# Performance work log

Hardware: AMD Instinct MI355X
Metric: run time of the kernel (lower is better)

The kernel has to match this reference:

```python
import jax, jax.numpy as jnp
import numpy as np

DIM = 512
HEADS = 8
DH = DIM // HEADS          # 64
M = DIM // 2               # 256 landmarks
ITERS = 6
KSZ = 33                   # residual depthwise conv kernel
LN_EPS = 1e-5
SCALE = DH ** -0.5


def setup_inputs() -> dict:
    key = jax.random.key(0)
    ks = jax.random.split(key, 5)
    b, n = 2, 8192
    x = jax.random.normal(ks[0], (b, n, DIM), jnp.float32)
    ln_g = jnp.ones((DIM,), jnp.float32)
    ln_b = jnp.zeros((DIM,), jnp.float32)
    sc = 1.0 / np.sqrt(DIM)
    W_qkv = (jax.random.normal(ks[1], (DIM, 3 * DIM), jnp.float32) * sc)
    W_out = (jax.random.normal(ks[2], (DIM, DIM), jnp.float32) * sc)
    b_out = jnp.zeros((DIM,), jnp.float32)
    conv_w = jax.random.normal(ks[3], (HEADS, 1, KSZ, 1), jnp.float32) * (1.0 / np.sqrt(KSZ))
    return dict(x=x, ln_g=ln_g, ln_b=ln_b, W_qkv=W_qkv, W_out=W_out, b_out=b_out, conv_w=conv_w)


def _pinv_iter(a, iters=ITERS):
    # Moore-Penrose pseudo-inverse via Newton-Schulz (lucidrains variant)
    abs_a = jnp.abs(a)
    col = abs_a.sum(-1)
    row = abs_a.sum(-2)
    z = jnp.swapaxes(a, -1, -2) / (jnp.max(col) * jnp.max(row))
    I = jnp.eye(a.shape[-1], dtype=a.dtype)
    for _ in range(iters):
        az = a @ z
        z = 0.25 * z @ (13 * I - az @ (15 * I - az @ (7 * I - az)))
    return z


def _nystrom_attention(xn, W_qkv, conv_w, W_out, b_out):
    b, n, _ = xn.shape
    qkv = xn @ W_qkv                                   # [b,n,3*dim]
    q, k, v = jnp.split(qkv, 3, axis=-1)
    to_heads = lambda t: t.reshape(b, n, HEADS, DH).transpose(0, 2, 1, 3)  # [b,h,n,d]
    q, k, v = to_heads(q), to_heads(k), to_heads(v)
    q = q * SCALE

    # landmarks: mean over contiguous groups of size l = n // M (n divisible by M)
    l = n // M
    q_l = q.reshape(b, HEADS, M, l, DH).sum(3) / l     # [b,h,M,d]
    k_l = k.reshape(b, HEADS, M, l, DH).sum(3) / l

    sim1 = jnp.einsum('bhnd,bhmd->bhnm', q, k_l)       # [b,h,n,M]
    sim2 = jnp.einsum('bhid,bhjd->bhij', q_l, k_l)     # [b,h,M,M]
    sim3 = jnp.einsum('bhmd,bhnd->bhmn', q_l, k)       # [b,h,M,n]

    attn1 = jax.nn.softmax(sim1, axis=-1)
    attn2 = jax.nn.softmax(sim2, axis=-1)
    attn3 = jax.nn.softmax(sim3, axis=-1)
    attn2_inv = _pinv_iter(attn2)

    out = (attn1 @ attn2_inv) @ (attn3 @ v)            # [b,h,n,d]

    # depthwise conv residual over sequence dim, per head (Conv2d kernel (33,1), groups=heads)
    pad = KSZ // 2
    res = jax.lax.conv_general_dilated(
        v, conv_w, window_strides=(1, 1), padding=((pad, pad), (0, 0)),
        dimension_numbers=('NCHW', 'OIHW', 'NCHW'), feature_group_count=HEADS)
    out = out + res

    out = out.transpose(0, 2, 1, 3).reshape(b, n, DIM)
    return out @ W_out + b_out


def reference(x, ln_g, ln_b, W_qkv, W_out, b_out, conv_w):
    mu = x.mean(-1, keepdims=True)
    var = x.var(-1, keepdims=True)
    xn = (x - mu) / jnp.sqrt(var + LN_EPS) * ln_g + ln_b
    return xn + _nystrom_attention(xn, W_qkv, conv_w, W_out, b_out)
```

## Files before the change

kernel.cpp:

```cpp
#include <hip/hip_runtime.h>

typedef unsigned short u16;
typedef short bh8 __attribute__((ext_vector_type(8)));
typedef float f32x4 __attribute__((ext_vector_type(4)));

#define NSEQ 8192
#define ALOFF 1048576
#define KVLOFF 262144
#define NSPLIT 8

__device__ __forceinline__ float b2f(u16 u){
  union { unsigned int u32; float f; } v; v.u32 = ((unsigned int)u) << 16; return v.f;
}
__device__ __forceinline__ u16 f2b(float f){
  union { float f; unsigned int u32; } v; v.f = f;
  unsigned int r = (v.u32 + 0x7FFFu + ((v.u32 >> 16) & 1u)) >> 16;
  return (u16)r;
}
__device__ __forceinline__ void glds16(const u16* g, u16* l){
  __builtin_amdgcn_global_load_lds((const __attribute__((address_space(1))) unsigned int*)g,
                                   (__attribute__((address_space(3))) unsigned int*)l, 16, 0, 0);
}

__global__ __launch_bounds__(256) void setup_kernel(const void* g, const void* bta, const void* bo,
                                                    const void* cw, const void* wq, const void* wo,
                                                    u16* gb, u16* bb, u16* bob, u16* cwb,
                                                    u16* wqt, u16* wot,
                                                    unsigned* flag, float* colsum){
  int f32 = (((const u16*)g)[0] != 0x3F80u);
  long tid = (long)blockIdx.x*256 + threadIdx.x;
  long nth = (long)gridDim.x*256;
  if(tid==0){ *flag = (unsigned)f32; }
  for(long i=tid;i<4096;i+=nth) colsum[i]=0.f;
  for(long i=tid;i<512;i+=nth) gb[i]  = f32 ? f2b(((const float*)g)[i])   : ((const u16*)g)[i];
  for(long i=tid;i<512;i+=nth) bb[i]  = f32 ? f2b(((const float*)bta)[i]) : ((const u16*)bta)[i];
  for(long i=tid;i<512;i+=nth) bob[i] = f32 ? f2b(((const float*)bo)[i])  : ((const u16*)bo)[i];
  for(long i=tid;i<264;i+=nth) cwb[i] = f32 ? f2b(((const float*)cw)[i])  : ((const u16*)cw)[i];
  for(long i=tid;i<786432;i+=nth){
    long n = i>>9, k = i&511;
    wqt[i] = f32 ? f2b(((const float*)wq)[k*1536+n]) : ((const u16*)wq)[k*1536+n];
  }
  for(long i=tid;i<262144;i+=nth){
    long n = i>>9, k = i&511;
    wot[i] = f32 ? f2b(((const float*)wo)[k*512+n]) : ((const u16*)wo)[k*512+n];
  }
}

__global__ __launch_bounds__(256) void ln_kernel(const void* xv, const unsigned* flag,
                                                 const u16* g, const u16* bta, u16* xn){
  int f32 = (*flag != 0u);
  long base = (long)blockIdx.x * 512;
  int t = threadIdx.x;
  float v0, v1;
  if(f32){ v0 = ((const float*)xv)[base+t]; v1 = ((const float*)xv)[base+256+t]; }
  else   { v0 = b2f(((const u16*)xv)[base+t]); v1 = b2f(((const u16*)xv)[base+256+t]); }
  float s = v0 + v1, sq = v0*v0 + v1*v1;
  #pragma unroll
  for(int k=1;k<64;k<<=1){ s += __shfl_xor(s,k,64); sq += __shfl_xor(sq,k,64); }
  __shared__ float s4[4], q4[4];
  if((t&63)==0){ s4[t>>6]=s; q4[t>>6]=sq; }
  __syncthreads();
  s = s4[0]+s4[1]+s4[2]+s4[3];
  sq = q4[0]+q4[1]+q4[2]+q4[3];
  float mu = s * (1.f/512.f);
  float var = sq * (1.f/512.f) - mu*mu;
  float inv = rsqrtf(var + 1e-5f);
  xn[base + t]       = f2b((v0-mu)*inv*b2f(g[t])     + b2f(bta[t]));
  xn[base + 256 + t] = f2b((v1-mu)*inv*b2f(g[t+256]) + b2f(bta[t+256]));
}

struct G128 {
  const u16 *A, *Bt; u16* C;
  const u16 *bias, *resid;
  const unsigned* oflag;
  int lda, ldb, ldc, ldr, K;
};
__global__ __launch_bounds__(256) void gemm128_kernel(G128 p){
  __shared__ u16 Ah[128][32];
  __shared__ u16 Bh[128][32];
  int t = threadIdx.x;
  int n0 = blockIdx.x*128, m0 = blockIdx.y*128;
  int w = t>>6, lane = t&63, l15 = lane&15, quad = lane>>4;
  int mw = (w>>1)*64, nw = (w&1)*64;
  int srow = lane>>2;
  int schunk = ((lane&3) ^ ((srow>>1)&3))*8;
  int cs = (quad ^ ((l15>>1)&3))*8;
  f32x4 acc[4][4];
  #pragma unroll
  for(int i=0;i<4;i++)
    #pragma unroll
    for(int j=0;j<4;j++)
      #pragma unroll
      for(int k=0;k<4;k++) acc[i][j][k]=0.f;

  for(int kk=0; kk<p.K; kk+=32){
    __syncthreads();
    glds16(p.A  + (long)(m0+32*w+srow)*p.lda    + kk + schunk, &Ah[32*w][0]);
    glds16(p.A  + (long)(m0+32*w+16+srow)*p.lda + kk + schunk, &Ah[32*w+16][0]);
    glds16(p.Bt + (long)(n0+32*w+srow)*p.ldb    + kk + schunk, &Bh[32*w][0]);
    glds16(p.Bt + (long)(n0+32*w+16+srow)*p.ldb + kk + schunk, &Bh[32*w+16][0]);
    __syncthreads();
    bh8 av[4], bv[4];
    #pragma unroll
    for(int mi=0;mi<4;mi++) av[mi] = *(const bh8*)&Ah[mw + mi*16 + l15][cs];
    #pragma unroll
    for(int ni=0;ni<4;ni++) bv[ni] = *(const bh8*)&Bh[nw + ni*16 + l15][cs];
    #pragma unroll
    for(int mi=0;mi<4;mi++)
      #pragma unroll
      for(int ni=0;ni<4;ni++)
        acc[mi][ni] = __builtin_amdgcn_mfma_f32_16x16x32_bf16(av[mi], bv[ni], acc[mi][ni], 0,0,0);
  }
  int f32o = p.oflag ? (int)(*p.oflag) : 0;
  #pragma unroll
  for(int mi=0;mi<4;mi++)
    #pragma unroll
    for(int ni=0;ni<4;ni++)
      #pragma unroll
      for(int r=0;r<4;r++){
        int row = m0 + mw + mi*16 + quad*4 + r;
        int col = n0 + nw + ni*16 + l15;
        float v = acc[mi][ni][r];
        if(p.bias)  v += b2f(p.bias[col]);
        if(p.resid) v += b2f(p.resid[(long)row*p.ldr + col]);
        long coff = (long)row*p.ldc + col;
        if(p.oflag){
          if(f32o) ((float*)p.C)[coff] = v; else p.C[coff] = f2b(v);
        } else p.C[coff] = f2b(v);
      }
}

__global__ __launch_bounds__(64) void landmark_kernel(const u16* qkv, u16* ql, u16* kl){
  int m = blockIdx.x, bh = blockIdx.y;
  int b = bh>>3, h = bh&7;
  int d = threadIdx.x;
  long base = ((long)b*NSEQ + (long)m*32)*1536 + h*64 + d;
  float sq=0.f, sk=0.f;
  for(int i=0;i<32;i++){
    sq += b2f(qkv[base + (long)i*1536]);
    sk += b2f(qkv[base + (long)i*1536 + 512]);
  }
  long o = ((long)bh*256 + m)*64 + d;
  ql[o] = f2b(sq * (1.f/32.f) * 0.125f);
  kl[o] = f2b(sk * (1.f/32.f));
}

__global__ __launch_bounds__(256) void sim2_kernel(const u16* ql, const u16* kl,
                                                   u16* ab, float* colsum){
  int mt = blockIdx.x, bh = blockIdx.y;
  __shared__ u16 qlds[64][72];
  __shared__ u16 klds[256][72];
  int t = threadIdx.x, w = t>>6, lane = t&63, l15 = lane&15, quad = lane>>4;
  {
    int r = t>>2, c = (t&3)*16;
    const u16* src = ql + (long)bh*16384 + (long)(mt*64 + r)*64 + c;
    *(uint4*)&qlds[r][c]   = *(const uint4*)src;
    *(uint4*)&qlds[r][c+8] = *(const uint4*)(src+8);
    #pragma unroll
    for(int pss=0; pss<4; pss++){
      int kr = pss*64 + r;
      const u16* ks = kl + (long)bh*16384 + (long)kr*64 + c;
      *(uint4*)&klds[kr][c]   = *(const uint4*)ks;
      *(uint4*)&klds[kr][c+8] = *(const uint4*)(ks+8);
    }
  }
  __syncthreads();
  f32x4 acc[16];
  #pragma unroll
  for(int i=0;i<16;i++)
    #pragma unroll
    for(int j=0;j<4;j++) acc[i][j]=0.f;
  #pragma unroll
  for(int g=0; g<16; g++)
    #pragma unroll
    for(int kk=0; kk<64; kk+=32){
      bh8 a  = *(const bh8*)&qlds[w*16+l15][kk+quad*8];
      bh8 bb = *(const bh8*)&klds[g*16+l15][kk+quad*8];
      acc[g] = __builtin_amdgcn_mfma_f32_16x16x32_bf16(a, bb, acc[g], 0,0,0);
    }
  #pragma unroll
  for(int r=0;r<4;r++){
    float m = -3.0e38f;
    #pragma unroll
    for(int g=0;g<16;g++) m = fmaxf(m, acc[g][r]);
    #pragma unroll
    for(int k=1;k<16;k<<=1) m = fmaxf(m, __shfl_xor(m,k,16));
    float s = 0.f;
    #pragma unroll
    for(int g=0;g<16;g++){ float e = __expf(acc[g][r]-m); acc[g][r]=e; s+=e; }
    #pragma unroll
    for(int k=1;k<16;k<<=1) s += __shfl_xor(s,k,16);
    float inv = 1.f/s;
    #pragma unroll
    for(int g=0;g<16;g++) acc[g][r] *= inv;
  }
  long bbase = (long)bh*65536;
  #pragma unroll
  for(int g=0;g<16;g++){
    float ps = 0.f;
    #pragma unroll
    for(int r=0;r<4;r++){
      int row = mt*64 + w*16 + quad*4 + r;
      int col = g*16 + l15;
      float pv = acc[g][r];
      u16 h = f2b(pv);
      ab[bbase + (long)row*256 + col] = h;
      ab[ALOFF + bbase + (long)row*256 + col] = f2b(pv - b2f(h));
      ps += pv;
    }
    ps += __shfl_xor(ps, 16);
    ps += __shfl_xor(ps, 32);
    if(quad==0) atomicAdd(&colsum[bh*256 + g*16 + l15], ps);
  }
}

__global__ __launch_bounds__(256) void pinv_init_kernel(const u16* ah, const float* colsum, u16* zh){
  int tile = blockIdx.x, bh = blockIdx.y;
  int tx = tile&3, ty = tile>>2;
  __shared__ u16 th[64][72], tl[64][72];
  __shared__ float red[4];
  int t = threadIdx.x;
  float mc = 0.f;
  for(int i=t;i<4096;i+=256) mc = fmaxf(mc, colsum[i]);
  #pragma unroll
  for(int k=1;k<64;k<<=1) mc = fmaxf(mc, __shfl_xor(mc,k,64));
  if((t&63)==0) red[t>>6]=mc;
  int r = t>>2, c = (t&3)*16;
  const u16* src = ah + (long)bh*65536 + (long)(ty*64 + r)*256 + tx*64 + c;
  *(uint4*)&th[r][c]   = *(const uint4*)src;
  *(uint4*)&th[r][c+8] = *(const uint4*)(src+8);
  *(uint4*)&tl[r][c]   = *(const uint4*)(src+ALOFF);
  *(uint4*)&tl[r][c+8] = *(const uint4*)(src+ALOFF+8);
  __syncthreads();
  float dinv = 1.f/fmaxf(fmaxf(red[0],red[1]), fmaxf(red[2],red[3]));
  u16 oh[16], ol[16];
  #pragma unroll
  for(int jj=0;jj<16;jj++){
    float v = (b2f(th[c+jj][r]) + b2f(tl[c+jj][r])) * dinv;
    u16 h = f2b(v);
    oh[jj] = h; ol[jj] = f2b(v - b2f(h));
  }
  u16* dst = zh + (long)bh*65536 + (long)(tx*64 + r)*256 + ty*64 + c;
  *(uint4*)dst     = *(uint4*)oh;
  *(uint4*)(dst+8) = *(uint4*)(oh+8);
  *(uint4*)(dst+ALOFF)   = *(uint4*)ol;
  *(uint4*)(dst+ALOFF+8) = *(uint4*)(ol+8);
}

struct NSG { const u16 *A, *B; u16 *Ch, *Cl, *C2h, *C2l; float alpha, beta, alpha2, beta2; };
__global__ __launch_bounds__(256) void ns_gemm_kernel(NSG p){
  __shared__ u16 Ah[64][40], Al[64][40], Bh[64][40], Bl[64][40];
  int t = threadIdx.x;
  long boff = (long)blockIdx.z*65536;
  int n0 = blockIdx.x*64, m0 = blockIdx.y*64;
  int w = t>>6, lane = t&63, l15 = lane&15, quad = lane>>4;
  int ar = t>>2, ac = (t&3)*8;
  int bk = t>>3, bn = (t&7)*8;
  f32x4 acc[4];
  #pragma unroll
  for(int i=0;i<4;i++)
    #pragma unroll
    for(int j=0;j<4;j++) acc[i][j]=0.f;
  for(int kk=0; kk<256; kk+=32){
    __syncthreads();
    *(uint4*)&Ah[ar][ac] = *(const uint4*)(p.A + boff + (long)(m0+ar)*256 + kk + ac);
    *(uint4*)&Al[ar][ac] = *(const uint4*)(p.A + ALOFF + boff + (long)(m0+ar)*256 + kk + ac);
    u16 th[8], tl[8];
    *(uint4*)th = *(const uint4*)(p.B + boff + (long)(kk+bk)*256 + n0 + bn);
    *(uint4*)tl = *(const uint4*)(p.B + ALOFF + boff + (long)(kk+bk)*256 + n0 + bn);
    #pragma unroll
    for(int j=0;j<8;j++){ Bh[bn+j][bk] = th[j]; Bl[bn+j][bk] = tl[j]; }
    __syncthreads();
    bh8 a  = *(const bh8*)&Ah[w*16+l15][quad*8];
    bh8 al = *(const bh8*)&Al[w*16+l15][quad*8];
    #pragma unroll
    for(int ct=0; ct<4; ct++){
      bh8 b  = *(const bh8*)&Bh[ct*16+l15][quad*8];
      bh8 bl = *(const bh8*)&Bl[ct*16+l15][quad*8];
      acc[ct] = __builtin_amdgcn_mfma_f32_16x16x32_bf16(a,  b,  acc[ct], 0,0,0);
      acc[ct] = __builtin_amdgcn_mfma_f32_16x16x32_bf16(a,  bl, acc[ct], 0,0,0);
      acc[ct] = __builtin_amdgcn_mfma_f32_16x16x32_bf16(al, b,  acc[ct], 0,0,0);
    }
  }
  #pragma unroll
  for(int ct=0; ct<4; ct++)
    #pragma unroll
    for(int r=0;r<4;r++){
      int col = n0 + ct*16 + l15;
      int row = m0 + w*16 + quad*4 + r;
      long coff = boff + (long)row*256 + col;
      float v = acc[ct][r];
      float v1 = p.alpha*v + ((row==col) ? p.beta : 0.f);
      u16 h = f2b(v1);
      p.Ch[coff] = h;
      p.Cl[coff] = f2b(v1 - b2f(h));
      if(p.C2h){
        float v2 = p.alpha2*v + ((row==col) ? p.beta2 : 0.f);
        u16 h2 = f2b(v2);
        p.C2h[coff] = h2;
        p.C2l[coff] = f2b(v2 - b2f(h2));
      }
    }
}

__global__ __launch_bounds__(256) void w2t_kernel(const u16* z, const u16* kvh, u16* w2t){
  __shared__ u16 Ah[64][40], Al[64][40], Bh[64][40], Bl[64][40];
  int t = threadIdx.x;
  int bh = blockIdx.z;
  int m0 = blockIdx.y*64;
  long za = (long)bh*65536;
  long kb = (long)bh*16384;
  int w = t>>6, lane = t&63, l15 = lane&15, quad = lane>>4;
  int ar = t>>2, ac = (t&3)*8;
  int bk = t>>3, bn = (t&7)*8;
  f32x4 acc[4];
  #pragma unroll
  for(int i=0;i<4;i++)
    #pragma unroll
    for(int j=0;j<4;j++) acc[i][j]=0.f;
  for(int kk=0; kk<256; kk+=32){
    __syncthreads();
    *(uint4*)&Ah[ar][ac] = *(const uint4*)(z + za + (long)(m0+ar)*256 + kk + ac);
    *(uint4*)&Al[ar][ac] = *(const uint4*)(z + ALOFF + za + (long)(m0+ar)*256 + kk + ac);
    u16 th[8], tl[8];
    *(uint4*)th = *(const uint4*)(kvh + kb + (long)(kk+bk)*64 + bn);
    *(uint4*)tl = *(const uint4*)(kvh + KVLOFF + kb + (long)(kk+bk)*64 + bn);
    #pragma unroll
    for(int j=0;j<8;j++){ Bh[bn+j][bk] = th[j]; Bl[bn+j][bk] = tl[j]; }
    __syncthreads();
    bh8 a  = *(const bh8*)&Ah[w*16+l15][quad*8];
    bh8 al = *(const bh8*)&Al[w*16+l15][quad*8];
    #pragma unroll
    for(int ct=0; ct<4; ct++){
      bh8 b  = *(const bh8*)&Bh[ct*16+l15][quad*8];
      bh8 bl = *(const bh8*)&Bl[ct*16+l15][quad*8];
      acc[ct] = __builtin_amdgcn_mfma_f32_16x16x32_bf16(a,  b,  acc[ct], 0,0,0);
      acc[ct] = __builtin_amdgcn_mfma_f32_16x16x32_bf16(a,  bl, acc[ct], 0,0,0);
      acc[ct] = __builtin_amdgcn_mfma_f32_16x16x32_bf16(al, b,  acc[ct], 0,0,0);
    }
  }
  #pragma unroll
  for(int ct=0; ct<4; ct++)
    #pragma unroll
    for(int r=0;r<4;r++){
      int col = ct*16 + l15;
      int row = m0 + w*16 + quad*4 + r;
      w2t[kb + (long)col*256 + row] = f2b(acc[ct][r]);
    }
}

__global__ __launch_bounds__(256) void attn3f_kernel(const u16* ql, const u16* qkv,
                                                     float* opart, float* mpart, float* lpart){
  int s = blockIdx.x, mt = blockIdx.y, bh = blockIdx.z;
  int b = bh>>3, h = bh&7;
  __shared__ u16 qlds[64][72];
  __shared__ u16 Kh[128][72];
  __shared__ u16 Vt[64][136];
  __shared__ u16 plds[64][136];
  int t = threadIdx.x, w = t>>6, lane = t&63, l15 = lane&15, quad = lane>>4;
  {
    int r = t>>2, c = (t&3)*16;
    const u16* src = ql + (long)bh*16384 + (long)(mt*64 + r)*64 + c;
    *(uint4*)&qlds[r][c]   = *(const uint4*)src;
    *(uint4*)&qlds[r][c+8] = *(const uint4*)(src+8);
  }
  float mrun[4], lrun[4];
  #pragma unroll
  for(int r=0;r<4;r++){ mrun[r] = -3.0e38f; lrun[r] = 0.f; }
  f32x4 O[4];
  #pragma unroll
  for(int i=0;i<4;i++)
    #pragma unroll
    for(int j=0;j<4;j++) O[i][j]=0.f;

  for(int ch=0; ch<8; ch++){
    long n0 = (long)s*1024 + ch*128;
    __syncthreads();
    #pragma unroll
    for(int pss=0; pss<4; pss++){
      int r = pss*32 + (t>>3), c = (t&7)*8;
      const u16* ksrc = qkv + 512 + ((long)b*NSEQ + n0 + r)*1536 + h*64 + c;
      *(uint4*)&Kh[r][c] = *(const uint4*)ksrc;
      u16 tv[8];
      *(uint4*)tv = *(const uint4*)(ksrc + 512);
      #pragma unroll
      for(int j=0;j<8;j++) Vt[c+j][r] = tv[j];
    }
    __syncthreads();
    f32x4 sc[8];
    #pragma unroll
    for(int i=0;i<8;i++)
      #pragma unroll
      for(int j=0;j<4;j++) sc[i][j]=0.f;
    #pragma unroll
    for(int g=0; g<8; g++)
      #pragma unroll
      for(int kk=0; kk<64; kk+=32){
        bh8 a  = *(const bh8*)&qlds[w*16+l15][kk+quad*8];
        bh8 bb = *(const bh8*)&Kh[g*16+l15][kk+quad*8];
        sc[g] = __builtin_amdgcn_mfma_f32_16x16x32_bf16(a, bb, sc[g], 0,0,0);
      }
    #pragma unroll
    for(int r=0;r<4;r++){
      float cm = -3.0e38f;
      #pragma unroll
      for(int g=0;g<8;g++) cm = fmaxf(cm, sc[g][r]);
      #pragma unroll
      for(int k=1;k<16;k<<=1) cm = fmaxf(cm, __shfl_xor(cm,k,16));
      float nm = fmaxf(mrun[r], cm);
      float alpha = __expf(mrun[r]-nm);
      mrun[r] = nm;
      float psum = 0.f;
      #pragma unroll
      for(int g=0;g<8;g++){ float e = __expf(sc[g][r]-nm); sc[g][r]=e; psum+=e; }
      #pragma unroll
      for(int k=1;k<16;k<<=1) psum += __shfl_xor(psum,k,16);
      lrun[r] = lrun[r]*alpha + psum;
      #pragma unroll
      for(int ct=0;ct<4;ct++) O[ct][r] *= alpha;
    }
    #pragma unroll
    for(int g=0;g<8;g++)
      #pragma unroll
      for(int r=0;r<4;r++)
        plds[w*16 + quad*4 + r][g*16 + l15] = f2b(sc[g][r]);
    __syncthreads();
    #pragma unroll
    for(int kk=0; kk<128; kk+=32){
      bh8 a = *(const bh8*)&plds[w*16+l15][kk+quad*8];
      #pragma unroll
      for(int ct=0; ct<4; ct++){
        bh8 bb = *(const bh8*)&Vt[ct*16+l15][kk+quad*8];
        O[ct] = __builtin_amdgcn_mfma_f32_16x16x32_bf16(a, bb, O[ct], 0,0,0);
      }
    }
  }
  long rbase = (long)(s*16 + bh)*256 + mt*64 + w*16;
  #pragma unroll
  for(int ct=0; ct<4; ct++)
    #pragma unroll
    for(int r=0;r<4;r++)
      opart[(rbase + quad*4 + r)*64 + ct*16 + l15] = O[ct][r];
  if(l15==0){
    #pragma unroll
    for(int r=0;r<4;r++){
      mpart[rbase + quad*4 + r] = mrun[r];
      lpart[rbase + quad*4 + r] = lrun[r];
    }
  }
}

__global__ __launch_bounds__(256) void kvcomb_kernel(const float* opart, const float* mpart,
                                                     const float* lpart, u16* kvh){
  long i = (long)blockIdx.x*256 + threadIdx.x;
  int col = (int)(i & 63);
  long rb = i >> 6;
  float M = -3.0e38f;
  #pragma unroll
  for(int s=0;s<NSPLIT;s++) M = fmaxf(M, mpart[(long)s*4096 + rb]);
  float num = 0.f, den = 0.f;
  #pragma unroll
  for(int s=0;s<NSPLIT;s++){
    float e = __expf(mpart[(long)s*4096 + rb] - M);
    den += e * lpart[(long)s*4096 + rb];
    num += e * opart[((long)s*4096 + rb)*64 + col];
  }
  float v = num/den;
  u16 h = f2b(v);
  kvh[i] = h;
  kvh[KVLOFF + i] = f2b(v - b2f(h));
}

__global__ __launch_bounds__(256) void attn1_kernel(const u16* qkv, const u16* kl,
                                                    const u16* w2t, u16* oh2){
  int bh = blockIdx.y, b = bh>>3, h = bh&7;
  int n0 = blockIdx.x*64;
  __shared__ u16 qlds[64][72];
  __shared__ u16 klds[64][72];
  __shared__ u16 plds[64][264];
  __shared__ u16 w2lds[64][72];
  int t = threadIdx.x, w = t>>6, lane = t&63, l15 = lane&15, quad = lane>>4;
  {
    int r = t>>2, c = (t&3)*16;
    const u16* src = qkv + ((long)b*NSEQ + n0 + r)*1536 + h*64 + c;
    *(uint4*)&qlds[r][c]   = *(const uint4*)src;
    *(uint4*)&qlds[r][c+8] = *(const uint4*)(src+8);
  }
  f32x4 acc[16];
  #pragma unroll
  for(int i=0;i<16;i++)
    #pragma unroll
    for(int j=0;j<4;j++) acc[i][j]=0.f;
  const u16* klb = kl + (long)bh*16384;
  for(int nt=0; nt<4; nt++){
    __syncthreads();
    {
      int r = t>>2, c = (t&3)*16;
      const u16* src = klb + (long)(nt*64 + r)*64 + c;
      *(uint4*)&klds[r][c]   = *(const uint4*)src;
      *(uint4*)&klds[r][c+8] = *(const uint4*)(src+8);
    }
    __syncthreads();
    #pragma unroll
    for(int kk=0; kk<64; kk+=32){
      bh8 a = *(const bh8*)&qlds[w*16+l15][kk+quad*8];
      #pragma unroll
      for(int ct=0; ct<4; ct++){
        bh8 bb = *(const bh8*)&klds[ct*16+l15][kk+quad*8];
        acc[nt*4+ct] = __builtin_amdgcn_mfma_f32_16x16x32_bf16(a, bb, acc[nt*4+ct], 0,0,0);
      }
    }
  }
  float linv[4];
  #pragma unroll
  for(int g=0; g<16; g++)
    #pragma unroll
    for(int r=0;r<4;r++) acc[g][r] *= 0.125f;
  #pragma unroll
  for(int r=0;r<4;r++){
    float m = -3.0e38f;
    #pragma unroll
    for(int g=0;g<16;g++) m = fmaxf(m, acc[g][r]);
    #pragma unroll
    for(int k=1;k<16;k<<=1) m = fmaxf(m, __shfl_xor(m,k,16));
    float s = 0.f;
    #pragma unroll
    for(int g=0;g<16;g++){ float e = __expf(acc[g][r]-m); acc[g][r]=e; s+=e; }
    #pragma unroll
    for(int k=1;k<16;k<<=1) s += __shfl_xor(s,k,16);
    linv[r] = 1.f/s;
  }
  #pragma unroll
  for(int g=0;g<16;g++)
    #pragma unroll
    for(int r=0;r<4;r++)
      plds[w*16 + quad*4 + r][g*16 + l15] = f2b(acc[g][r]*linv[r]);
  f32x4 acc2[4];
  #pragma unroll
  for(int i=0;i<4;i++)
    #pragma unroll
    for(int j=0;j<4;j++) acc2[i][j]=0.f;
  const u16* w2b = w2t + (long)bh*16384;
  for(int kc=0; kc<4; kc++){
    __syncthreads();
    {
      int r = t>>2, c = (t&3)*16;
      const u16* src = w2b + (long)r*256 + kc*64 + c;
      *(uint4*)&w2lds[r][c]   = *(const uint4*)src;
      *(uint4*)&w2lds[r][c+8] = *(const uint4*)(src+8);
    }
    __syncthreads();
    #pragma unroll
    for(int kk=0; kk<64; kk+=32){
      bh8 a = *(const bh8*)&plds[w*16+l15][kc*64+kk+quad*8];
      #pragma unroll
      for(int ct=0; ct<4; ct++){
        bh8 bb = *(const bh8*)&w2lds[ct*16+l15][kk+quad*8];
        acc2[ct] = __builtin_amdgcn_mfma_f32_16x16x32_bf16(a, bb, acc2[ct], 0,0,0);
      }
    }
  }
  #pragma unroll
  for(int ct=0; ct<4; ct++)
    #pragma unroll
    for(int r=0;r<4;r++){
      int nrow = n0 + w*16 + quad*4 + r;
      int d = ct*16 + l15;
      oh2[((long)b*NSEQ + nrow)*512 + h*64 + d] = f2b(acc2[ct][r]);
    }
}

__global__ __launch_bounds__(256) void conv_add_kernel(const u16* qkv, const u16* cw, u16* oh2){
  int bh = blockIdx.y, b = bh>>3, h = bh&7;
  int n0 = blockIdx.x*256;
  __shared__ u16 vlds[288][64];
  __shared__ float wsh[33];
  int t = threadIdx.x;
  if(t<33) wsh[t] = b2f(cw[h*33 + t]);
  for(int r = t>>2; r<288; r+=64){
    int c = (t&3)*16;
    int n = n0 - 16 + r;
    if(n>=0 && n<NSEQ){
      const u16* src = qkv + ((long)b*NSEQ + n)*1536 + 1024 + h*64 + c;
      *(uint4*)&vlds[r][c]   = *(const uint4*)src;
      *(uint4*)&vlds[r][c+8] = *(const uint4*)(src+8);
    } else {
      uint4 zz; zz.x=zz.y=zz.z=zz.w=0u;
      *(uint4*)&vlds[r][c]   = zz;
      *(uint4*)&vlds[r][c+8] = zz;
    }
  }
  __syncthreads();
  int d = t&63, sub = t>>6;
  for(int i=0;i<64;i++){
    int nloc = sub + i*4;
    float s = 0.f;
    #pragma unroll
    for(int j=0;j<33;j++) s += b2f(vlds[nloc+j][d]) * wsh[j];
    long o = ((long)b*NSEQ + n0 + nloc)*512 + h*64 + d;
    oh2[o] = f2b(b2f(oh2[o]) + s);
  }
}

extern "C" void kernel_launch(void* const* d_in, const int* in_sizes, int n_in,
                              void* d_out, int out_size, void* d_ws, size_t ws_size,
                              hipStream_t stream){
  char* wsp = (char*)d_ws;
  size_t off = 0;
  auto alloc = [&](size_t bytes)->char*{
    char* p = wsp + off; off = (off + bytes + 255) & ~(size_t)255; return p;
  };
  u16* gb   = (u16*)alloc(1024);
  u16* bb   = (u16*)alloc(1024);
  u16* bob  = (u16*)alloc(1024);
  u16* cwb  = (u16*)alloc(1024);
  u16* wqt  = (u16*)alloc(1572864);
  u16* wot  = (u16*)alloc(524288);
  unsigned* flag = (unsigned*)alloc(256);
  float* colsum = (float*)alloc(16384);
  u16*   xn   = (u16*)alloc(16777216);
  u16*   qkv  = (u16*)alloc(50331648);
  u16*   ql   = (u16*)alloc(524288);
  u16*   kl   = (u16*)alloc(524288);
  u16*   ab   = (u16*)alloc(4194304);
  u16*   zA   = (u16*)alloc(4194304);
  u16*   zB   = (u16*)alloc(4194304);
  u16*   az   = (u16*)alloc(4194304);
  u16*   t1b  = (u16*)alloc(4194304);
  u16*   t2b  = (u16*)alloc(4194304);
  u16*   kvb  = (u16*)alloc(1048576);
  u16*   w2t  = (u16*)alloc(524288);
  u16*   oh2  = (u16*)alloc(16777216);
  float* opart= (float*)alloc(8388608);
  float* mpart= (float*)alloc(131072);
  float* lpart= (float*)alloc(131072);

  setup_kernel<<<dim3(1024), 256, 0, stream>>>(d_in[1], d_in[2], d_in[5], d_in[6],
                                               d_in[3], d_in[4],
                                               gb, bb, bob, cwb, wqt, wot, flag, colsum);
  ln_kernel<<<dim3(16384), 256, 0, stream>>>(d_in[0], flag, gb, bb, xn);
  { G128 p{}; p.A=xn; p.Bt=wqt; p.C=qkv; p.lda=512; p.ldb=512; p.ldc=1536; p.K=512;
    gemm128_kernel<<<dim3(12,128,1), 256, 0, stream>>>(p); }
  landmark_kernel<<<dim3(256,16), dim3(64), 0, stream>>>(qkv, ql, kl);
  sim2_kernel<<<dim3(4,16), 256, 0, stream>>>(ql, kl, ab, colsum);
  pinv_init_kernel<<<dim3(16,16), 256, 0, stream>>>(ab, colsum, zA);
  { u16* zc = zA; u16* zn = zB;
    for(int it=0; it<6; it++){
      { NSG q{ab, zc, az, az+ALOFF, t1b, t1b+ALOFF, 1.f, 0.f, -1.f, 7.f};
        ns_gemm_kernel<<<dim3(4,4,16), 256, 0, stream>>>(q); }
      { NSG q{az, t1b, t2b, t2b+ALOFF, nullptr, nullptr, -1.f, 15.f, 0.f, 0.f};
        ns_gemm_kernel<<<dim3(4,4,16), 256, 0, stream>>>(q); }
      { NSG q{az, t2b, t1b, t1b+ALOFF, nullptr, nullptr, -1.f, 13.f, 0.f, 0.f};
        ns_gemm_kernel<<<dim3(4,4,16), 256, 0, stream>>>(q); }
      { NSG q{zc, t1b, zn, zn+ALOFF, nullptr, nullptr, 0.25f, 0.f, 0.f, 0.f};
        ns_gemm_kernel<<<dim3(4,4,16), 256, 0, stream>>>(q); }
      u16* tmp = zc; zc = zn; zn = tmp;
    } }
  attn3f_kernel<<<dim3(NSPLIT,4,16), 256, 0, stream>>>(ql, qkv, opart, mpart, lpart);
  kvcomb_kernel<<<dim3(1024), 256, 0, stream>>>(opart, mpart, lpart, kvb);
  w2t_kernel<<<dim3(1,4,16), 256, 0, stream>>>(zA, kvb, w2t);
  attn1_kernel<<<dim3(128,16), 256, 0, stream>>>(qkv, kl, w2t, oh2);
  conv_add_kernel<<<dim3(32,16), 256, 0, stream>>>(qkv, cwb, oh2);
  { G128 p{}; p.A=oh2; p.Bt=wot; p.C=(u16*)d_out; p.bias=bob; p.resid=xn; p.oflag=flag;
    p.lda=512; p.ldb=512; p.ldc=512; p.ldr=512; p.K=512;
    gemm128_kernel<<<dim3(4,128,1), 256, 0, stream>>>(p); }
}
```

Measured before the change: 631.4 us.

## Restructure Newton-Schulz pinv iterations, stage full-K tiles, fuse conv residual into attn1

The pseudo-inverse loop now carries y = a@z forward as y_new = 0.25 * y @ t3 and computes it in the same batched launch as z_new. This replaces four dependent GEMM launches per iteration with three, and that kernel also produces the next 7I - y term. The remaining NS GEMMs use a new kernel that loads the whole 256-deep K panel into LDS once, removing per-step barriers at the cost of much larger shared memory. The depthwise conv residual is fused into the attn1 epilogue, which drops a separate kernel and a read-modify-write pass over oh2. The recurrence for y can drift numerically from recomputing a@z directly.

New measurement: 588.0 us. 6.9% less time.

```diff
diff --git a/kernel.cpp b/kernel.cpp
--- a/kernel.cpp
+++ b/kernel.cpp
@@ -247,36 +247,43 @@
   *(uint4*)(dst+ALOFF+8) = *(uint4*)(ol+8);
 }
 
-struct NSG { const u16 *A, *B; u16 *Ch, *Cl, *C2h, *C2l; float alpha, beta, alpha2, beta2; };
-__global__ __launch_bounds__(256) void ns_gemm_kernel(NSG p){
-  __shared__ u16 Ah[64][40], Al[64][40], Bh[64][40], Bl[64][40];
+struct NS2 { const u16 *A, *B; u16 *Ch, *Cl, *C2h, *C2l; float alpha, beta, alpha2, beta2; };
+__global__ __launch_bounds__(256) void ns2_kernel(NS2 p){
+  __shared__ u16 Ah[64][264], Al[64][264];
+  __shared__ u16 Bt[64][264], Blt[64][264];
   int t = threadIdx.x;
   long boff = (long)blockIdx.z*65536;
   int n0 = blockIdx.x*64, m0 = blockIdx.y*64;
+  #pragma unroll
+  for(int i=0;i<8;i++){
+    int idx = (i*256+t)*8, r = idx>>8, c = idx&255;
+    *(uint4*)&Ah[r][c] = *(const uint4*)(p.A + boff + (long)(m0+r)*256 + c);
+    *(uint4*)&Al[r][c] = *(const uint4*)(p.A + ALOFF + boff + (long)(m0+r)*256 + c);
+  }
+  #pragma unroll
+  for(int i=0;i<8;i++){
+    int idx = (i*256+t)*8, k = idx>>6, n = idx&63;
+    u16 th[8], tl[8];
+    *(uint4*)th = *(const uint4*)(p.B + boff + (long)k*256 + n0 + n);
+    *(uint4*)tl = *(const uint4*)(p.B + ALOFF + boff + (long)k*256 + n0 + n);
+    #pragma unroll
+    for(int j=0;j<8;j++){ Bt[n+j][k] = th[j]; Blt[n+j][k] = tl[j]; }
+  }
+  __syncthreads();
   int w = t>>6, lane = t&63, l15 = lane&15, quad = lane>>4;
-  int ar = t>>2, ac = (t&3)*8;
-  int bk = t>>3, bn = (t&7)*8;
   f32x4 acc[4];
   #pragma unroll
   for(int i=0;i<4;i++)
     #pragma unroll
     for(int j=0;j<4;j++) acc[i][j]=0.f;
+  #pragma unroll
   for(int kk=0; kk<256; kk+=32){
-    __syncthreads();
-    *(uint4*)&Ah[ar][ac] = *(const uint4*)(p.A + boff + (long)(m0+ar)*256 + kk + ac);
-    *(uint4*)&Al[ar][ac] = *(const uint4*)(p.A + ALOFF + boff + (long)(m0+ar)*256 + kk + ac);
-    u16 th[8], tl[8];
-    *(uint4*)th = *(const uint4*)(p.B + boff + (long)(kk+bk)*256 + n0 + bn);
-    *(uint4*)tl = *(const uint4*)(p.B + ALOFF + boff + (long)(kk+bk)*256 + n0 + bn);
-    #pragma unroll
-    for(int j=0;j<8;j++){ Bh[bn+j][bk] = th[j]; Bl[bn+j][bk] = tl[j]; }
-    __syncthreads();
-    bh8 a  = *(const bh8*)&Ah[w*16+l15][quad*8];
-    bh8 al = *(const bh8*)&Al[w*16+l15][quad*8];
+    bh8 a  = *(const bh8*)&Ah[w*16+l15][kk+quad*8];
+    bh8 al = *(const bh8*)&Al[w*16+l15][kk+quad*8];
     #pragma unroll
     for(int ct=0; ct<4; ct++){
-      bh8 b  = *(const bh8*)&Bh[ct*16+l15][quad*8];
-      bh8 bl = *(const bh8*)&Bl[ct*16+l15][quad*8];
+      bh8 b  = *(const bh8*)&Bt[ct*16+l15][kk+quad*8];
+      bh8 bl = *(const bh8*)&Blt[ct*16+l15][kk+quad*8];
       acc[ct] = __builtin_amdgcn_mfma_f32_16x16x32_bf16(a,  b,  acc[ct], 0,0,0);
       acc[ct] = __builtin_amdgcn_mfma_f32_16x16x32_bf16(a,  bl, acc[ct], 0,0,0);
       acc[ct] = __builtin_amdgcn_mfma_f32_16x16x32_bf16(al, b,  acc[ct], 0,0,0);
@@ -303,6 +310,64 @@
     }
 }
 
+struct NSZ { const u16 *zc, *yc, *t3; u16 *zn, *yn, *t1; };
+__global__ __launch_bounds__(256) void nsz_kernel(NSZ p){
+  __shared__ u16 Ah[64][40], Al[64][40], Bh[64][40], Bl[64][40];
+  int t = threadIdx.x;
+  int bz = blockIdx.z, half = bz>>4, bh = bz&15;
+  long boff = (long)bh*65536;
+  int n0 = blockIdx.x*64, m0 = blockIdx.y*64;
+  const u16* A = half ? p.yc : p.zc;
+  u16* C = half ? p.yn : p.zn;
+  int w = t>>6, lane = t&63, l15 = lane&15, quad = lane>>4;
+  int ar = t>>2, ac = (t&3)*8;
+  int bk = t>>3, bn = (t&7)*8;
+  f32x4 acc[4];
+  #pragma unroll
+  for(int i=0;i<4;i++)
+    #pragma unroll
+    for(int j=0;j<4;j++) acc[i][j]=0.f;
+  for(int kk=0; kk<256; kk+=32){
+    __syncthreads();
+    *(uint4*)&Ah[ar][ac] = *(const uint4*)(A + boff + (long)(m0+ar)*256 + kk + ac);
+    *(uint4*)&Al[ar][ac] = *(const uint4*)(A + ALOFF + boff + (long)(m0+ar)*256 + kk + ac);
+    u16 th[8], tl[8];
+    *(uint4*)th = *(const uint4*)(p.t3 + boff + (long)(kk+bk)*256 + n0 + bn);
+    *(uint4*)tl = *(const uint4*)(p.t3 + ALOFF + boff + (long)(kk+bk)*256 + n0 + bn);
+    #pragma unroll
+    for(int j=0;j<8;j++){ Bh[bn+j][bk] = th[j]; Bl[bn+j][bk] = tl[j]; }
+    __syncthreads();
+    bh8 a  = *(const bh8*)&Ah[w*16+l15][quad*8];
+    bh8 al = *(const bh8*)&Al[w*16+l15][quad*8];
+    #pragma unroll
+    for(int ct=0; ct<4; ct++){
+      bh8 b  = *(const bh8*)&Bh[ct*16+l15][quad*8];
+      bh8 bl = *(const bh8*)&Bl[ct*16+l15][quad*8];
+      acc[ct] = __builtin_amdgcn_mfma_f32_16x16x32_bf16(a,  b,  acc[ct], 0,0,0);
+      acc[ct] = __builtin_amdgcn_mfma_f32_16x16x32_bf16(a,  bl, acc[ct], 0,0,0);
+      acc[ct] = __builtin_amdgcn_mfma_f32_16x16x32_bf16(al, b,  acc[ct], 0,0,0);
+    }
+  }
+  #pragma unroll
+  for(int ct=0; ct<4; ct++)
+    #pragma unroll
+    for(int r=0;r<4;r++){
+      int col = n0 + ct*16 + l15;
+      int row = m0 + w*16 + quad*4 + r;
+      long coff = boff + (long)row*256 + col;
+      float v = 0.25f*acc[ct][r];
+      u16 h = f2b(v);
+      C[coff] = h;
+      C[ALOFF + coff] = f2b(v - b2f(h));
+      if(half){
+        float v2 = ((row==col) ? 7.f : 0.f) - v;
+        u16 h2 = f2b(v2);
+        p.t1[coff] = h2;
+        p.t1[ALOFF + coff] = f2b(v2 - b2f(h2));
+      }
+    }
+}
+
 __global__ __launch_bounds__(256) void w2t_kernel(const u16* z, const u16* kvh, u16* w2t){
   __shared__ u16 Ah[64][40], Al[64][40], Bh[64][40], Bl[64][40];
   int t = threadIdx.x;
@@ -471,21 +536,36 @@
   kvh[KVLOFF + i] = f2b(v - b2f(h));
 }
 
-__global__ __launch_bounds__(256) void attn1_kernel(const u16* qkv, const u16* kl,
-                                                    const u16* w2t, u16* oh2){
+__global__ __launch_bounds__(256) void attn1c_kernel(const u16* qkv, const u16* kl,
+                                                     const u16* w2t, const u16* cw, u16* oh2){
   int bh = blockIdx.y, b = bh>>3, h = bh&7;
   int n0 = blockIdx.x*64;
   __shared__ u16 qlds[64][72];
   __shared__ u16 klds[64][72];
   __shared__ u16 plds[64][264];
   __shared__ u16 w2lds[64][72];
+  __shared__ u16 vlds[96][72];
+  __shared__ float wsh[33];
   int t = threadIdx.x, w = t>>6, lane = t&63, l15 = lane&15, quad = lane>>4;
+  if(t<33) wsh[t] = b2f(cw[h*33 + t]);
   {
     int r = t>>2, c = (t&3)*16;
     const u16* src = qkv + ((long)b*NSEQ + n0 + r)*1536 + h*64 + c;
     *(uint4*)&qlds[r][c]   = *(const uint4*)src;
     *(uint4*)&qlds[r][c+8] = *(const uint4*)(src+8);
   }
+  #pragma unroll
+  for(int i=0;i<3;i++){
+    int idx = i*256 + t;
+    int r = idx>>3, c = (idx&7)*8;
+    int n = n0 - 16 + r;
+    if(n>=0 && n<NSEQ){
+      *(uint4*)&vlds[r][c] = *(const uint4*)(qkv + ((long)b*NSEQ + n)*1536 + 1024 + h*64 + c);
+    } else {
+      uint4 zz; zz.x=zz.y=zz.z=zz.w=0u;
+      *(uint4*)&vlds[r][c] = zz;
+    }
+  }
   f32x4 acc[16];
   #pragma unroll
   for(int i=0;i<16;i++)
@@ -564,42 +644,13 @@
   for(int ct=0; ct<4; ct++)
     #pragma unroll
     for(int r=0;r<4;r++){
-      int nrow = n0 + w*16 + quad*4 + r;
+      int nloc = w*16 + quad*4 + r;
       int d = ct*16 + l15;
-      oh2[((long)b*NSEQ + nrow)*512 + h*64 + d] = f2b(acc2[ct][r]);
-    }
-}
-
-__global__ __launch_bounds__(256) void conv_add_kernel(const u16* qkv, const u16* cw, u16* oh2){
-  int bh = blockIdx.y, b = bh>>3, h = bh&7;
-  int n0 = blockIdx.x*256;
-  __shared__ u16 vlds[288][64];
-  __shared__ float wsh[33];
-  int t = threadIdx.x;
-  if(t<33) wsh[t] = b2f(cw[h*33 + t]);
-  for(int r = t>>2; r<288; r+=64){
-    int c = (t&3)*16;
-    int n = n0 - 16 + r;
-    if(n>=0 && n<NSEQ){
-      const u16* src = qkv + ((long)b*NSEQ + n)*1536 + 1024 + h*64 + c;
-      *(uint4*)&vlds[r][c]   = *(const uint4*)src;
-      *(uint4*)&vlds[r][c+8] = *(const uint4*)(src+8);
-    } else {
-      uint4 zz; zz.x=zz.y=zz.z=zz.w=0u;
-      *(uint4*)&vlds[r][c]   = zz;
-      *(uint4*)&vlds[r][c+8] = zz;
-    }
-  }
-  __syncthreads();
-  int d = t&63, sub = t>>6;
-  for(int i=0;i<64;i++){
-    int nloc = sub + i*4;
-    float s = 0.f;
-    #pragma unroll
-    for(int j=0;j<33;j++) s += b2f(vlds[nloc+j][d]) * wsh[j];
-    long o = ((long)b*NSEQ + n0 + nloc)*512 + h*64 + d;
-    oh2[o] = f2b(b2f(oh2[o]) + s);
-  }
+      float s = 0.f;
+      #pragma unroll
+      for(int j=0;j<33;j++) s += b2f(vlds[nloc+j][d]) * wsh[j];
+      oh2[((long)b*NSEQ + n0 + nloc)*512 + h*64 + d] = f2b(acc2[ct][r] + s);
+    }
 }
 
 extern "C" void kernel_launch(void* const* d_in, const int* in_sizes, int n_in,
@@ -625,9 +676,11 @@
   u16*   ab   = (u16*)alloc(4194304);
   u16*   zA   = (u16*)alloc(4194304);
   u16*   zB   = (u16*)alloc(4194304);
-  u16*   az   = (u16*)alloc(4194304);
+  u16*   yA   = (u16*)alloc(4194304);
+  u16*   yB   = (u16*)alloc(4194304);
   u16*   t1b  = (u16*)alloc(4194304);
   u16*   t2b  = (u16*)alloc(4194304);
+  u16*   t3b  = (u16*)alloc(4194304);
   u16*   kvb  = (u16*)alloc(1048576);
   u16*   w2t  = (u16*)alloc(524288);
   u16*   oh2  = (u16*)alloc(16777216);
@@ -644,23 +697,23 @@
   landmark_kernel<<<dim3(256,16), dim3(64), 0, stream>>>(qkv, ql, kl);
   sim2_kernel<<<dim3(4,16), 256, 0, stream>>>(ql, kl, ab, colsum);
   pinv_init_kernel<<<dim3(16,16), 256, 0, stream>>>(ab, colsum, zA);
-  { u16* zc = zA; u16* zn = zB;
-    for(int it=0; it<6; it++){
-      { NSG q{ab, zc, az, az+ALOFF, t1b, t1b+ALOFF, 1.f, 0.f, -1.f, 7.f};
-        ns_gemm_kernel<<<dim3(4,4,16), 256, 0, stream>>>(q); }
-      { NSG q{az, t1b, t2b, t2b+ALOFF, nullptr, nullptr, -1.f, 15.f, 0.f, 0.f};
-        ns_gemm_kernel<<<dim3(4,4,16), 256, 0, stream>>>(q); }
-      { NSG q{az, t2b, t1b, t1b+ALOFF, nullptr, nullptr, -1.f, 13.f, 0.f, 0.f};
-        ns_gemm_kernel<<<dim3(4,4,16), 256, 0, stream>>>(q); }
-      { NSG q{zc, t1b, zn, zn+ALOFF, nullptr, nullptr, 0.25f, 0.f, 0.f, 0.f};
-        ns_gemm_kernel<<<dim3(4,4,16), 256, 0, stream>>>(q); }
-      u16* tmp = zc; zc = zn; zn = tmp;
-    } }
+  { NS2 q{ab, zA, yA, yA+ALOFF, t1b, t1b+ALOFF, 1.f, 0.f, -1.f, 7.f};
+    ns2_kernel<<<dim3(4,4,16), 256, 0, stream>>>(q); }
+  u16 *zc=zA, *zn=zB, *yc=yA, *yn=yB;
+  for(int it=0; it<6; it++){
+    { NS2 q{yc, t1b, t2b, t2b+ALOFF, nullptr, nullptr, -1.f, 15.f, 0.f, 0.f};
+      ns2_kernel<<<dim3(4,4,16), 256, 0, stream>>>(q); }
+    { NS2 q{yc, t2b, t3b, t3b+ALOFF, nullptr, nullptr, -1.f, 13.f, 0.f, 0.f};
+      ns2_kernel<<<dim3(4,4,16), 256, 0, stream>>>(q); }
+    { NSZ q{zc, yc, t3b, zn, yn, t1b};
+      nsz_kernel<<<dim3(4,4,32), 256, 0, stream>>>(q); }
+    u16* tz=zc; zc=zn; zn=tz;
+    u16* ty=yc; yc=yn; yn=ty;
+  }
   attn3f_kernel<<<dim3(NSPLIT,4,16), 256, 0, stream>>>(ql, qkv, opart, mpart, lpart);
   kvcomb_kernel<<<dim3(1024), 256, 0, stream>>>(opart, mpart, lpart, kvb);
-  w2t_kernel<<<dim3(1,4,16), 256, 0, stream>>>(zA, kvb, w2t);
-  attn1_kernel<<<dim3(128,16), 256, 0, stream>>>(qkv, kl, w2t, oh2);
-  conv_add_kernel<<<dim3(32,16), 256, 0, stream>>>(qkv, cwb, oh2);
+  w2t_kernel<<<dim3(1,4,16), 256, 0, stream>>>(zc, kvb, w2t);
+  attn1c_kernel<<<dim3(128,16), 256, 0, stream>>>(qkv, kl, w2t, cwb, oh2);
   { G128 p{}; p.A=oh2; p.Bt=wot; p.C=(u16*)d_out; p.bias=bob; p.resid=xn; p.oflag=flag;
     p.lda=512; p.ldb=512; p.ldc=512; p.ldr=512; p.K=512;
     gemm128_kernel<<<dim3(4,128,1), 256, 0, stream>>>(p); }
```
